# Kernel optimization log

Measured on AMD Instinct MI355X. Metric: run time of the kernel, lower is better.

The kernel has to match this reference:

```python
import jax, jax.numpy as jnp
import numpy as np

B1, B2, R, L, D, H = 48, 48, 36, 30, 1024, 4
EPS = 1e-8


def _l2norm(x):
    return x / (jnp.sqrt(jnp.sum(x * x, axis=-1, keepdims=True)) + EPS)


def _summary_attn(x, w1, b1, w2, b2):
    # x: (B1,B2,N,D). MLP scores -> softmax over N -> weighted mean over H heads.
    h = jax.nn.relu(jnp.einsum('abnd,ed->abne', x, w1) + b1)
    s = jnp.einsum('abne,he->abnh', h, w2) + b2          # (B1,B2,N,H)
    p = jax.nn.softmax(jnp.swapaxes(s, -1, -2), axis=-1)  # (B1,B2,H,N)
    w = jnp.einsum('abhn,abnd->abhd', p, x)               # (B1,B2,H,D)
    return w.mean(axis=-2)                                # (B1,B2,D)


def setup_inputs() -> dict:
    key = jax.random.key(0)
    ks = jax.random.split(key, 12)
    r = np.sqrt(6.0) / np.sqrt(D + D)  # xavier uniform as in init_weights
    return {
        'v1': jax.random.normal(ks[0], (B1, R, D), dtype=jnp.float32),
        'v2': jax.random.normal(ks[1], (B2, L, D), dtype=jnp.float32),
        'w_img': jax.random.uniform(ks[2], (D, D), jnp.float32, -r, r),
        'w_txt': jax.random.uniform(ks[3], (D, D), jnp.float32, -r, r),
        'w1a': jax.random.normal(ks[4], (D, D), jnp.float32) * 0.02,
        'b1a': jnp.zeros((D,), jnp.float32),
        'w2a': jax.random.normal(ks[5], (H, D), jnp.float32) * 0.02,
        'b2a': jnp.zeros((H,), jnp.float32),
        'w1b': jax.random.normal(ks[6], (D, D), jnp.float32) * 0.02,
        'b1b': jnp.zeros((D,), jnp.float32),
        'w2b': jax.random.normal(ks[7], (H, D), jnp.float32) * 0.02,
        'b2b': jnp.zeros((H,), jnp.float32),
    }


def reference(v1, v2, w_img, w_txt, w1a, b1a, w2a, b2a, w1b, b1b, w2b, b2b):
    d = v1.shape[-1]
    inv_sqrt_d = np.float32(1.0 / np.sqrt(d))
    k1 = jnp.einsum('ard,ed->are', v1, w_img)  # (B1,R,D)
    k2 = jnp.einsum('bld,ed->ble', v2, w_txt)  # (B2,L,D)

    # qkv_attention(k2, k1, v1): queries=words, keys/values=regions
    s1 = jnp.einsum('bld,ard->ablr', k2, k1) * inv_sqrt_d   # (B1,B2,L,R)
    p1 = jax.nn.softmax(s1, axis=-1)
    fused_v2 = jnp.einsum('ablr,ard->abld', p1, v1)         # weighted_v1 -> fused_v2

    # qkv_attention(k1, k2, v2): queries=regions, keys/values=words
    s2 = jnp.einsum('ard,bld->abrl', k1, k2) * inv_sqrt_d   # (B1,B2,R,L)
    p2 = jax.nn.softmax(s2, axis=-1)
    fused_v1 = jnp.einsum('abrl,bld->abrd', p2, v2)         # weighted_v2 -> fused_v1

    co_v1 = _l2norm(_summary_attn(fused_v1, w1a, b1a, w2a, b2a))
    co_v2 = _l2norm(_summary_attn(fused_v2, w1b, b1b, w2b, b2b))
    return jnp.sum(co_v1 * co_v2, axis=-1)  # (B1,B2) score matrix
```

## Files before the change

### kernel.cpp

```cpp
#include <hip/hip_runtime.h>

#define D 1024
#define NB1 48
#define NB2 48
#define RR 36
#define LL 30
#define NH 4

typedef short bf16x8 __attribute__((ext_vector_type(8)));
typedef float f32x4 __attribute__((ext_vector_type(4)));
typedef float f32x2 __attribute__((ext_vector_type(2)));
typedef unsigned short u16x8 __attribute__((ext_vector_type(8)));

#define MFMA16(a, b, c) __builtin_amdgcn_mfma_f32_16x16x32_bf16(a, b, c, 0, 0, 0)

__device__ __forceinline__ unsigned short f2bf(float x) {
  unsigned u = __float_as_uint(x);
  u += 0x7FFF + ((u >> 16) & 1);
  return (unsigned short)(u >> 16);
}
__device__ __forceinline__ float bf2f(unsigned short h) {
  return __uint_as_float(((unsigned)h) << 16);
}
__device__ __forceinline__ void split8(const float* v, bf16x8& h8, bf16x8& l8) {
  u16x8 hi, lo;
#pragma unroll
  for (int i = 0; i < 8; ++i) {
    unsigned short h = f2bf(v[i]);
    hi[i] = h;
    lo[i] = f2bf(v[i] - bf2f(h));
  }
  h8 = __builtin_bit_cast(bf16x8, hi);
  l8 = __builtin_bit_cast(bf16x8, lo);
}
__device__ __forceinline__ f32x2 shflx2(f32x2 v, int m) {
  double d = __builtin_bit_cast(double, v);
  d = __shfl_xor(d, m);
  return __builtin_bit_cast(f32x2, d);
}

__device__ __forceinline__ void conv_body(const float* __restrict__ X,
                                          unsigned short* __restrict__ out,
                                          int rows, int g) {
  const int lane = threadIdx.x & 63;
  const int tile = g >> 5, kc = g & 31;
  const int row = tile * 16 + (lane & 15);
  const int k = kc * 32 + (lane >> 4) * 8;
  float v[8];
  if (row < rows) {
    const float4* s = (const float4*)(X + (size_t)row * 1024 + k);
    float4 x0 = s[0], x1 = s[1];
    v[0] = x0.x; v[1] = x0.y; v[2] = x0.z; v[3] = x0.w;
    v[4] = x1.x; v[5] = x1.y; v[6] = x1.z; v[7] = x1.w;
  } else {
#pragma unroll
    for (int i = 0; i < 8; ++i) v[i] = 0.f;
  }
  bf16x8 hi, lo;
  split8(v, hi, lo);
  bf16x8* o = (bf16x8*)(out + (size_t)g * 1024 + lane * 8);
  o[0] = hi;
  o[64] = lo;
}

__global__ __launch_bounds__(256) void conv6(
    const float* __restrict__ v1, const float* __restrict__ v2,
    const float* __restrict__ wimg, const float* __restrict__ wtxt,
    const float* __restrict__ w1a, const float* __restrict__ w1b,
    const float* __restrict__ w2a, const float* __restrict__ w2b,
    unsigned short* v1f, unsigned short* v2f, unsigned short* wimgf,
    unsigned short* wtxtf, unsigned short* w1af, unsigned short* w1bf,
    float4* __restrict__ w2at, float4* __restrict__ w2bt) {
  if (blockIdx.y == 0 && blockIdx.x < 4) {
    int col = blockIdx.x * 256 + threadIdx.x;
    w2at[col] = make_float4(w2a[col], w2a[1024 + col], w2a[2048 + col], w2a[3072 + col]);
    w2bt[col] = make_float4(w2b[col], w2b[1024 + col], w2b[2048 + col], w2b[3072 + col]);
  }
  const float* X; unsigned short* O; int rows;
  switch (blockIdx.y) {
    case 0: X = v1; O = v1f; rows = 1728; break;
    case 1: X = v2; O = v2f; rows = 1440; break;
    case 2: X = wimg; O = wimgf; rows = 1024; break;
    case 3: X = wtxt; O = wtxtf; rows = 1024; break;
    case 4: X = w1a; O = w1af; rows = 1024; break;
    default: X = w1b; O = w1bf; rows = 1024; break;
  }
  const int tiles = (rows + 15) >> 4;
  const int g = blockIdx.x * 4 + (threadIdx.x >> 6);
  if (g >= tiles * 32) return;
  conv_body(X, O, rows, g);
}

__global__ __launch_bounds__(256) void convG(const float* __restrict__ G2a,
                                             const float* __restrict__ G1b,
                                             unsigned short* G2aF,
                                             unsigned short* G1bF) {
  const int t = threadIdx.x, lane = t & 63;
  const int bb = blockIdx.x >> 4;
  const int nt = ((blockIdx.x & 15) << 2) + (t >> 6);
  const int c = lane & 15, q = lane >> 4;
  if (blockIdx.y == 0) {
    float v[8];
#pragma unroll
    for (int j = 0; j < 8; ++j) {
      int l = q * 8 + j;
      v[j] = (l < LL) ? G2a[(size_t)(bb * LL + l) * D + nt * 16 + c] : 0.f;
    }
    bf16x8 hi, lo;
    split8(v, hi, lo);
    bf16x8* o = (bf16x8*)(G2aF + ((size_t)(bb * 64 + nt) * 2) * 512 + lane * 8);
    o[0] = hi;
    o[64] = lo;
  } else {
#pragma unroll
    for (int kc = 0; kc < 2; ++kc) {
      float v[8];
#pragma unroll
      for (int j = 0; j < 8; ++j) {
        int r = kc * 32 + q * 8 + j;
        v[j] = (r < RR) ? G1b[(size_t)(bb * RR + r) * D + nt * 16 + c] : 0.f;
      }
      bf16x8 hi, lo;
      split8(v, hi, lo);
      bf16x8* o = (bf16x8*)(G1bF + (((size_t)(bb * 64 + nt) * 2 + kc) * 2) * 512 + lane * 8);
      o[0] = hi;
      o[64] = lo;
    }
  }
}

#define LOAD_FRAGS(AH, AL, BH, BL)                                              \
  {                                                                             \
    _Pragma("unroll") for (int i = 0; i < 4; ++i) {                             \
      AH[i] = Af[ab[i]]; AL[i] = Af[ab[i] + 64]; ab[i] += 128;                  \
    }                                                                           \
    _Pragma("unroll") for (int j = 0; j < 4; ++j) {                             \
      BH[j] = Bf[bb[j]]; BL[j] = Bf[bb[j] + 64]; bb[j] += 128;                  \
    }                                                                           \
  }

#define MFMA_SET(AH, AL, BH, BL)                                                \
  _Pragma("unroll") for (int i = 0; i < 4; ++i)                                 \
      _Pragma("unroll") for (int j = 0; j < 4; ++j) {                           \
    acc[i][j] = MFMA16(AH[i], BH[j], acc[i][j]);                                \
    acc[i][j] = MFMA16(AL[i], BH[j], acc[i][j]);                                \
    acc[i][j] = MFMA16(AH[i], BL[j], acc[i][j]);                                \
  }

__device__ __forceinline__ void gemm2w_acc(const bf16x8* __restrict__ Af,
                                           const bf16x8* __restrict__ Bf,
                                           int Mtiles, int Ntiles,
                                           int mb, int nb, int lane,
                                           f32x4 (&acc)[4][4]) {
  int ab[4], bb[4];
#pragma unroll
  for (int i = 0; i < 4; ++i) {
    int tm = mb + i; if (tm > Mtiles - 1) tm = Mtiles - 1;
    ab[i] = tm * 4096 + lane;
    int tn = nb + i; if (tn > Ntiles - 1) tn = Ntiles - 1;
    bb[i] = tn * 4096 + lane;
  }
#pragma unroll
  for (int i = 0; i < 4; ++i)
#pragma unroll
    for (int j = 0; j < 4; ++j) acc[i][j] = (f32x4){0.f, 0.f, 0.f, 0.f};

  bf16x8 ahA[4], alA[4], bhA[4], blA[4];
  bf16x8 ahB[4], alB[4], bhB[4], blB[4];
  LOAD_FRAGS(ahA, alA, bhA, blA);
#pragma unroll 1
  for (int kc = 0; kc < 30; kc += 2) {
    LOAD_FRAGS(ahB, alB, bhB, blB);
    MFMA_SET(ahA, alA, bhA, blA);
    LOAD_FRAGS(ahA, alA, bhA, blA);
    MFMA_SET(ahB, alB, bhB, blB);
  }
  LOAD_FRAGS(ahB, alB, bhB, blB);
  MFMA_SET(ahA, alA, bhA, blA);
  MFMA_SET(ahB, alB, bhB, blB);
}

__device__ __forceinline__ void gemm2w_store_fp32(f32x4 (&acc)[4][4],
                                                  float* __restrict__ C,
                                                  int M, int N, float scale,
                                                  int mb, int nb, int lane) {
  const int c16 = lane & 15, q = lane >> 4;
#pragma unroll
  for (int i = 0; i < 4; ++i) {
#pragma unroll
    for (int reg = 0; reg < 4; ++reg) {
      int r = (mb + i) * 16 + q * 4 + reg;
      if (r < M) {
#pragma unroll
        for (int j = 0; j < 4; ++j) {
          int col = (nb + j) * 16 + c16;
          if (col < N) C[(size_t)r * N + col] = acc[i][j][reg] * scale;
        }
      }
    }
  }
}

__global__ __launch_bounds__(128) void proj_fused(
    const bf16x8* __restrict__ v1f, const bf16x8* __restrict__ v2f,
    const bf16x8* __restrict__ wimgf, const bf16x8* __restrict__ wtxtf,
    const bf16x8* __restrict__ w1af, const bf16x8* __restrict__ w1bf,
    float* G2a, float* G1b,
    unsigned short* k1f, unsigned short* k2f) {
  const int z = blockIdx.z;
  const int lane = threadIdx.x & 63;
  const int w = threadIdx.x >> 6;
  const int mb = blockIdx.y * 8 + w * 4;
  const int nb = blockIdx.x * 4;
  const bf16x8* Af = (z == 0 || z == 3) ? v1f : v2f;
  const bf16x8* Bf = (z == 0) ? wimgf : (z == 1) ? wtxtf : (z == 2) ? w1af : w1bf;
  const int Mt = (z == 0 || z == 3) ? 108 : 90;
  if ((int)blockIdx.y * 8 >= Mt) return;

  __shared__ __align__(16) float tlds[2][4][16][68];

  f32x4 acc[4][4];
  gemm2w_acc(Af, Bf, Mt, 64, mb, nb, lane, acc);

  if (z <= 1) {
    unsigned short* F = z ? k2f : k1f;
    const int c16 = lane & 15, q = lane >> 4;
#pragma unroll
    for (int i = 0; i < 4; ++i)
#pragma unroll
      for (int j = 0; j < 4; ++j)
#pragma unroll
        for (int reg = 0; reg < 4; ++reg)
          tlds[w][i][q * 4 + reg][j * 16 + c16] = acc[i][j][reg];
    __builtin_amdgcn_sched_barrier(0);
    const int r16 = lane & 15, q2 = lane >> 4;
#pragma unroll
    for (int i = 0; i < 4; ++i) {
      if (mb + i < Mt) {
#pragma unroll
        for (int kcl = 0; kcl < 2; ++kcl) {
          const float* rp = &tlds[w][i][r16][kcl * 32 + q2 * 8];
          float4 x0 = *(const float4*)rp;
          float4 x1 = *(const float4*)(rp + 4);
          float v[8];
          v[0] = x0.x; v[1] = x0.y; v[2] = x0.z; v[3] = x0.w;
          v[4] = x1.x; v[5] = x1.y; v[6] = x1.z; v[7] = x1.w;
          bf16x8 hi, lo;
          split8(v, hi, lo);
          size_t g = (size_t)(mb + i) * 32 + (nb >> 1) + kcl;
          bf16x8* o = (bf16x8*)(F + g * 1024 + lane * 8);
          o[0] = hi;
          o[64] = lo;
        }
      }
    }
  } else {
    float* C = (z == 2) ? G2a : G1b;
    const int M = (z == 2) ? 1440 : 1728;
    gemm2w_store_fp32(acc, C, M, 1024, 1.f, mb, nb, lane);
  }
}

__global__ __launch_bounds__(128) void cross_s(
    const bf16x8* __restrict__ k2f, const bf16x8* __restrict__ k1f,
    float* Sbuf) {
  const int lane = threadIdx.x & 63;
  const int w = threadIdx.x >> 6;
  const int mb = blockIdx.y * 8 + w * 4;
  const int nb = blockIdx.x * 4;
  f32x4 acc[4][4];
  gemm2w_acc(k2f, k1f, 90, 108, mb, nb, lane, acc);
  gemm2w_store_fp32(acc, Sbuf, 1440, 1728, 0.03125f, mb, nb, lane);
}

__global__ __launch_bounds__(256, 4) void pair_dir(
    const float* __restrict__ Sb,
    const bf16x8* __restrict__ G2aF, const bf16x8* __restrict__ G1bF,
    const float* __restrict__ b1a, const float4* __restrict__ w2at, const float* __restrict__ b2a,
    const float* __restrict__ b1b, const float4* __restrict__ w2bt, const float* __restrict__ b2b,
    float* __restrict__ U1buf, float* __restrict__ U2buf) {
  const int t = threadIdx.x, lane = t & 63, w = t >> 6;
  const int bx = blockIdx.x;
  int a, b, dir;
  if (bx < 576) {
    dir = 0;
    const int lo = bx & 7, i = bx >> 3;
    b = lo + 8 * (i % 6);
    a = (i / 6) * 4 + w;
  } else {
    dir = 1;
    const int bx2 = bx - 576;
    const int lo = bx2 & 7, i = bx2 >> 3;
    a = lo + 8 * (i % 6);
    b = (i / 6) * 4 + w;
  }
  const int c16 = lane & 15, q = lane >> 4;

  union WSM {
    struct { float p2s[36][36]; float sa[36][NH]; float qa[36]; } A;
    struct { float p1s[30][36]; float sbm[30][NH]; float qb[30]; } B;
  };
  __shared__ __align__(16) WSM sm[4];
  WSM& S = sm[w];

  const float* Sab = Sb + (size_t)(b * LL) * 1728 + a * RR;

  if (dir == 0) {
    if (lane < RR) { S.A.p2s[lane][30] = 0.f; S.A.p2s[lane][31] = 0.f; }
    __builtin_amdgcn_sched_barrier(0);
    for (int i = lane; i < LL * RR; i += 64) {
      int l = i / RR, r = i - l * RR;
      S.A.p2s[r][l] = Sab[(size_t)l * 1728 + r];
    }
    __builtin_amdgcn_sched_barrier(0);
    if (lane < RR) {
      const int r = lane;
      float m = -1e30f;
      for (int l = 0; l < LL; ++l) m = fmaxf(m, S.A.p2s[r][l]);
      float s = 0.f;
      for (int l = 0; l < LL; ++l) {
        float e = __expf(S.A.p2s[r][l] - m);
        S.A.p2s[r][l] = e;
        s += e;
      }
      float inv = 1.f / s;
      for (int l = 0; l < LL; ++l) S.A.p2s[r][l] *= inv;
    }
    __builtin_amdgcn_sched_barrier(0);

    bf16x8 pAh[3], pAl[3];
#pragma unroll
    for (int mt = 0; mt < 3; ++mt) {
      int rr = mt * 16 + c16;
      if (rr > RR - 1) rr = RR - 1;
      float v[8];
      const float* rp = &S.A.p2s[rr][q * 8];
      float4 x0 = *(const float4*)rp;
      float4 x1 = *(const float4*)(rp + 4);
      v[0] = x0.x; v[1] = x0.y; v[2] = x0.z; v[3] = x0.w;
      v[4] = x1.x; v[5] = x1.y; v[6] = x1.z; v[7] = x1.w;
      split8(v, pAh[mt], pAl[mt]);
    }

    f32x2 sc01[3][4], sc23[3][4];
#pragma unroll
    for (int mt = 0; mt < 3; ++mt)
#pragma unroll
      for (int reg = 0; reg < 4; ++reg) {
        sc01[mt][reg] = (f32x2){0.f, 0.f};
        sc23[mt][reg] = (f32x2){0.f, 0.f};
      }

    const bf16x8* gA = G2aF + (size_t)(b * 64) * 128 + lane;
#pragma unroll 2
    for (int it = 0; it < 64; ++it) {
      const bf16x8* gp = gA + (size_t)it * 128;
      bf16x8 Bh = gp[0], Bl = gp[64];
      const int col = it * 16 + c16;
      float4 wv = w2at[col];
      float bias = b1a[col];
      f32x2 w01 = {wv.x, wv.y}, w23 = {wv.z, wv.w};
#pragma unroll
      for (int mt = 0; mt < 3; ++mt) {
        f32x4 acc = {bias, bias, bias, bias};
        __builtin_amdgcn_s_setprio(1);
        acc = MFMA16(pAh[mt], Bh, acc);
        acc = MFMA16(pAl[mt], Bh, acc);
        acc = MFMA16(pAh[mt], Bl, acc);
        __builtin_amdgcn_s_setprio(0);
#pragma unroll
        for (int reg = 0; reg < 4; ++reg) {
          float hv = fmaxf(acc[reg], 0.f);
          f32x2 hv2 = {hv, hv};
          sc01[mt][reg] += hv2 * w01;
          sc23[mt][reg] += hv2 * w23;
        }
      }
    }
    f32x2 b01 = {b2a[0], b2a[1]}, b23 = {b2a[2], b2a[3]};
#pragma unroll
    for (int mt = 0; mt < 3; ++mt)
#pragma unroll
      for (int reg = 0; reg < 4; ++reg) {
        f32x2 v01 = sc01[mt][reg], v23 = sc23[mt][reg];
#pragma unroll
        for (int m = 1; m <= 8; m <<= 1) {
          v01 += shflx2(v01, m);
          v23 += shflx2(v23, m);
        }
        int row = mt * 16 + q * 4 + reg;
        if (c16 == 0 && row < RR) {
          f32x2* rp = (f32x2*)&S.A.sa[row][0];
          rp[0] = v01 + b01;
          rp[1] = v23 + b23;
        }
      }
    __builtin_amdgcn_sched_barrier(0);
    {
      const int h = q, i = c16;
      float x0 = S.A.sa[i][h];
      float x1 = S.A.sa[i + 16][h];
      float x2 = (i < 4) ? S.A.sa[i + 32][h] : -1e30f;
      float m = fmaxf(fmaxf(x0, x1), x2);
      m = fmaxf(m, __shfl_xor(m, 1));
      m = fmaxf(m, __shfl_xor(m, 2));
      m = fmaxf(m, __shfl_xor(m, 4));
      m = fmaxf(m, __shfl_xor(m, 8));
      float e0 = __expf(x0 - m), e1 = __expf(x1 - m);
      float e2 = (i < 4) ? __expf(x2 - m) : 0.f;
      float s = e0 + e1 + e2;
      s += __shfl_xor(s, 1);
      s += __shfl_xor(s, 2);
      s += __shfl_xor(s, 4);
      s += __shfl_xor(s, 8);
      float inv = 0.25f / s;
      float p0 = e0 * inv, p1 = e1 * inv, p2v = e2 * inv;
      p0 += __shfl_xor(p0, 16); p0 += __shfl_xor(p0, 32);
      p1 += __shfl_xor(p1, 16); p1 += __shfl_xor(p1, 32);
      p2v += __shfl_xor(p2v, 16); p2v += __shfl_xor(p2v, 32);
      if (q == 0) {
        S.A.qa[i] = p0;
        S.A.qa[i + 16] = p1;
        if (i < 4) S.A.qa[i + 32] = p2v;
      }
    }
    __builtin_amdgcn_sched_barrier(0);
    if (lane < LL) {
      const int l = lane;
      float x = 0.f;
      for (int r = 0; r < RR; ++r) x = fmaf(S.A.qa[r], S.A.p2s[r][l], x);
      U2buf[((size_t)b * 48 + a) * 32 + l] = x;
    }
  } else {
    for (int i = lane; i < LL * RR; i += 64) {
      int l = i / RR, r = i - l * RR;
      S.B.p1s[l][r] = Sab[(size_t)l * 1728 + r];
    }
    __builtin_amdgcn_sched_barrier(0);
    if (lane < LL) {
      const int l = lane;
      float m = -1e30f;
      for (int r = 0; r < RR; ++r) m = fmaxf(m, S.B.p1s[l][r]);
      float s = 0.f;
      for (int r = 0; r < RR; ++r) {
        float e = __expf(S.B.p1s[l][r] - m);
        S.B.p1s[l][r] = e;
        s += e;
      }
      float inv = 1.f / s;
      for (int r = 0; r < RR; ++r) S.B.p1s[l][r] *= inv;
    }
    __builtin_amdgcn_sched_barrier(0);

    bf16x8 pBh[2][2], pBl[2][2];
#pragma unroll
    for (int mt = 0; mt < 2; ++mt) {
      int rr = mt * 16 + c16;
      if (rr > LL - 1) rr = LL - 1;
      {
        float v[8];
        const float* rp = &S.B.p1s[rr][q * 8];
        float4 x0 = *(const float4*)rp;
        float4 x1 = *(const float4*)(rp + 4);
        v[0] = x0.x; v[1] = x0.y; v[2] = x0.z; v[3] = x0.w;
        v[4] = x1.x; v[5] = x1.y; v[6] = x1.z; v[7] = x1.w;
        split8(v, pBh[mt][0], pBl[mt][0]);
      }
      {
        float v[8];
#pragma unroll
        for (int j = 0; j < 8; ++j) {
          int r = 32 + q * 8 + j;
          v[j] = (r < RR) ? S.B.p1s[rr][r] : 0.f;
        }
        split8(v, pBh[mt][1], pBl[mt][1]);
      }
    }

    f32x2 sc01[2][4], sc23[2][4];
#pragma unroll
    for (int mt = 0; mt < 2; ++mt)
#pragma unroll
      for (int reg = 0; reg < 4; ++reg) {
        sc01[mt][reg] = (f32x2){0.f, 0.f};
        sc23[mt][reg] = (f32x2){0.f, 0.f};
      }

    const bf16x8* gB = G1bF + (size_t)(a * 64) * 256 + lane;
#pragma unroll 2
    for (int it = 0; it < 64; ++it) {
      const bf16x8* gp = gB + (size_t)it * 256;
      bf16x8 B0h = gp[0], B0l = gp[64], B1h = gp[128], B1l = gp[192];
      const int col = it * 16 + c16;
      float4 wv = w2bt[col];
      float bias = b1b[col];
      f32x2 w01 = {wv.x, wv.y}, w23 = {wv.z, wv.w};
#pragma unroll
      for (int mt = 0; mt < 2; ++mt) {
        f32x4 acc = {bias, bias, bias, bias};
        __builtin_amdgcn_s_setprio(1);
        acc = MFMA16(pBh[mt][0], B0h, acc);
        acc = MFMA16(pBl[mt][0], B0h, acc);
        acc = MFMA16(pBh[mt][0], B0l, acc);
        acc = MFMA16(pBh[mt][1], B1h, acc);
        acc = MFMA16(pBl[mt][1], B1h, acc);
        acc = MFMA16(pBh[mt][1], B1l, acc);
        __builtin_amdgcn_s_setprio(0);
#pragma unroll
        for (int reg = 0; reg < 4; ++reg) {
          float hv = fmaxf(acc[reg], 0.f);
          f32x2 hv2 = {hv, hv};
          sc01[mt][reg] += hv2 * w01;
          sc23[mt][reg] += hv2 * w23;
        }
      }
    }
    f32x2 b01 = {b2b[0], b2b[1]}, b23 = {b2b[2], b2b[3]};
#pragma unroll
    for (int mt = 0; mt < 2; ++mt)
#pragma unroll
      for (int reg = 0; reg < 4; ++reg) {
        f32x2 v01 = sc01[mt][reg], v23 = sc23[mt][reg];
#pragma unroll
        for (int m = 1; m <= 8; m <<= 1) {
          v01 += shflx2(v01, m);
          v23 += shflx2(v23, m);
        }
        int row = mt * 16 + q * 4 + reg;
        if (c16 == 0 && row < LL) {
          f32x2* rp = (f32x2*)&S.B.sbm[row][0];
          rp[0] = v01 + b01;
          rp[1] = v23 + b23;
        }
      }
    __builtin_amdgcn_sched_barrier(0);
    {
      const int h = q, i = c16;
      float x0 = S.B.sbm[i][h];
      float x1 = (i < 14) ? S.B.sbm[i + 16][h] : -1e30f;
      float m = fmaxf(x0, x1);
      m = fmaxf(m, __shfl_xor(m, 1));
      m = fmaxf(m, __shfl_xor(m, 2));
      m = fmaxf(m, __shfl_xor(m, 4));
      m = fmaxf(m, __shfl_xor(m, 8));
      float e0 = __expf(x0 - m);
      float e1 = (i < 14) ? __expf(x1 - m) : 0.f;
      float s = e0 + e1;
      s += __shfl_xor(s, 1);
      s += __shfl_xor(s, 2);
      s += __shfl_xor(s, 4);
      s += __shfl_xor(s, 8);
      float inv = 0.25f / s;
      float p0 = e0 * inv, p1 = e1 * inv;
      p0 += __shfl_xor(p0, 16); p0 += __shfl_xor(p0, 32);
      p1 += __shfl_xor(p1, 16); p1 += __shfl_xor(p1, 32);
      if (q == 0) {
        S.B.qb[i] = p0;
        if (i < 14) S.B.qb[i + 16] = p1;
      }
    }
    __builtin_amdgcn_sched_barrier(0);
    if (lane < RR) {
      const int r = lane;
      float x = 0.f;
      for (int l = 0; l < LL; ++l) x = fmaf(S.B.qb[l], S.B.p1s[l][r], x);
      U1buf[((size_t)a * 48 + b) * 40 + r] = x;
    }
  }
}

__global__ __launch_bounds__(256) void y_batch(
    const float* __restrict__ v1, const float* __restrict__ v2,
    const float* __restrict__ U1buf, const float* __restrict__ U2buf,
    float* __restrict__ YA, float* __restrict__ YB) {
  const int bb = blockIdx.x;
  const int col = blockIdx.z * 256 + threadIdx.x;
  __shared__ float us[48 * 40];
  float y[48];
#pragma unroll
  for (int i = 0; i < 48; ++i) y[i] = 0.f;
  if (blockIdx.y == 0) {
    for (int i = threadIdx.x; i < 48 * 32; i += 256) us[i] = U2buf[(size_t)bb * 1536 + i];
    __syncthreads();
    const float* V = v2 + (size_t)bb * LL * 1024 + col;
    for (int l = 0; l < LL; ++l) {
      float v = V[(size_t)l * 1024];
#pragma unroll
      for (int i = 0; i < 48; ++i) y[i] = fmaf(us[i * 32 + l], v, y[i]);
    }
    float* Yo = YA + (size_t)bb * 48 * 1024 + col;
#pragma unroll
    for (int i = 0; i < 48; ++i) Yo[(size_t)i * 1024] = y[i];
  } else {
    for (int i = threadIdx.x; i < 48 * 40; i += 256) us[i] = U1buf[(size_t)bb * 1920 + i];
    __syncthreads();
    const float* V = v1 + (size_t)bb * RR * 1024 + col;
    for (int r = 0; r < RR; ++r) {
      float v = V[(size_t)r * 1024];
#pragma unroll
      for (int i = 0; i < 48; ++i) y[i] = fmaf(us[i * 40 + r], v, y[i]);
    }
    float* Yo = YB + (size_t)bb * 48 * 1024 + col;
#pragma unroll
    for (int i = 0; i < 48; ++i) Yo[(size_t)i * 1024] = y[i];
  }
}

__global__ __launch_bounds__(256) void pair_final(
    const float* __restrict__ YA, const float* __restrict__ YB,
    float* __restrict__ out) {
  const int pair = blockIdx.x;
  const int a = pair / NB2;
  const int b = pair - a * NB2;
  const int t = threadIdx.x;
  const float4* ya = (const float4*)(YA + ((size_t)b * 48 + a) * 1024);
  const float4* yb = (const float4*)(YB + ((size_t)a * 48 + b) * 1024);
  float4 va = ya[t], vb = yb[t];
  float num = va.x * vb.x + va.y * vb.y + va.z * vb.z + va.w * vb.w;
  float n1 = va.x * va.x + va.y * va.y + va.z * va.z + va.w * va.w;
  float n2 = vb.x * vb.x + vb.y * vb.y + vb.z * vb.z + vb.w * vb.w;
#pragma unroll
  for (int off = 32; off; off >>= 1) {
    num += __shfl_down(num, off);
    n1 += __shfl_down(n1, off);
    n2 += __shfl_down(n2, off);
  }
  __shared__ float r3[3][4];
  if ((t & 63) == 0) {
    r3[0][t >> 6] = num; r3[1][t >> 6] = n1; r3[2][t >> 6] = n2;
  }
  __syncthreads();
  if (t == 0) {
    float nu = r3[0][0] + r3[0][1] + r3[0][2] + r3[0][3];
    float s1 = sqrtf(fmaxf(r3[1][0] + r3[1][1] + r3[1][2] + r3[1][3], 0.f));
    float s2 = sqrtf(fmaxf(r3[2][0] + r3[2][1] + r3[2][2] + r3[2][3], 0.f));
    out[pair] = nu / ((s1 + 1e-8f) * (s2 + 1e-8f));
  }
}

extern "C" void kernel_launch(void* const* d_in, const int* in_sizes, int n_in,
                              void* d_out, int out_size, void* d_ws, size_t ws_size,
                              hipStream_t stream) {
  const float* v1    = (const float*)d_in[0];
  const float* v2    = (const float*)d_in[1];
  const float* w_img = (const float*)d_in[2];
  const float* w_txt = (const float*)d_in[3];
  const float* w1a   = (const float*)d_in[4];
  const float* b1a   = (const float*)d_in[5];
  const float* w2a   = (const float*)d_in[6];
  const float* b2a   = (const float*)d_in[7];
  const float* w1b   = (const float*)d_in[8];
  const float* b1b   = (const float*)d_in[9];
  const float* w2b   = (const float*)d_in[10];
  const float* b2b   = (const float*)d_in[11];
  float* out = (float*)d_out;

  float* ws   = (float*)d_ws;
  float* k1   = ws;
  float* k2   = k1 + (size_t)1728 * 1024;
  float* G2a  = k2 + (size_t)1440 * 1024;
  float* G1b  = G2a + (size_t)1440 * 1024;
  float* Sbuf = G1b + (size_t)1728 * 1024;
  float* Cbuf = Sbuf + (size_t)1440 * 1728;
  float* g22  = Cbuf + (size_t)1440 * 1728;
  float* g11  = g22 + (size_t)48 * 900;
  (void)k1; (void)k2;

  unsigned short* fb    = (unsigned short*)(g11 + (size_t)48 * 1296);
  unsigned short* v1f   = fb;
  unsigned short* v2f   = v1f + (size_t)108 * 32768;
  unsigned short* k1f   = v2f + (size_t)92 * 32768;
  unsigned short* k2f   = k1f + (size_t)108 * 32768;
  unsigned short* wimgf = k2f + (size_t)92 * 32768;
  unsigned short* wtxtf = wimgf + (size_t)64 * 32768;
  unsigned short* w1af  = wtxtf + (size_t)64 * 32768;
  unsigned short* w1bf  = w1af + (size_t)64 * 32768;
  unsigned short* G2aF  = w1bf + (size_t)64 * 32768;
  unsigned short* G1bF  = G2aF + (size_t)48 * 65536;

  float4* w2at = (float4*)g22;
  float4* w2bt = w2at + 1024;

  float* U2buf = G2a;
  float* U1buf = U2buf + (size_t)48 * 48 * 32;
  float* YA = Cbuf;
  float* YB = (float*)k1f;

  conv6<<<dim3(864, 6), 256, 0, stream>>>(v1, v2, w_img, w_txt, w1a, w1b,
                                          w2a, w2b,
                                          v1f, v2f, wimgf, wtxtf, w1af, w1bf,
                                          w2at, w2bt);

  proj_fused<<<dim3(16, 14, 4), 128, 0, stream>>>(
      (const bf16x8*)v1f, (const bf16x8*)v2f, (const bf16x8*)wimgf,
      (const bf16x8*)wtxtf, (const bf16x8*)w1af, (const bf16x8*)w1bf,
      G2a, G1b, k1f, k2f);

  cross_s<<<dim3(27, 12), 128, 0, stream>>>(
      (const bf16x8*)k2f, (const bf16x8*)k1f, Sbuf);

  convG<<<dim3(768, 2), 256, 0, stream>>>(G2a, G1b, G2aF, G1bF);

  pair_dir<<<1152, 256, 0, stream>>>(
      Sbuf, (const bf16x8*)G2aF, (const bf16x8*)G1bF,
      b1a, w2at, b2a, b1b, w2bt, b2b, U1buf, U2buf);
  y_batch<<<dim3(48, 2, 4), 256, 0, stream>>>(v1, v2, U1buf, U2buf, YA, YB);
  pair_final<<<2304, 256, 0, stream>>>(YA, YB, out);
}
```

Before: 284.3 us.

## Move G projections out of projK and run them alongside the cross-score GEMM

Splits the fused projection kernel so the first launch only computes the k1/k2 projections. The G2a/G1b GEMMs, which do not depend on k1/k2, move into a second launch that also computes the cross-score S GEMM. This shortens the critical path: the S GEMM no longer waits behind the G GEMMs and shares a launch with them, filling the device better. The cost is a combined grid (27x14x3) in which many blocks exit early, plus some branch overhead.

```diff
diff --git a/kernel.cpp b/kernel.cpp
--- a/kernel.cpp
+++ b/kernel.cpp
@@ -201,20 +201,18 @@
   }
 }
 
-__global__ __launch_bounds__(128) void proj_fused(
+__global__ __launch_bounds__(128) void projK(
     const bf16x8* __restrict__ v1f, const bf16x8* __restrict__ v2f,
     const bf16x8* __restrict__ wimgf, const bf16x8* __restrict__ wtxtf,
-    const bf16x8* __restrict__ w1af, const bf16x8* __restrict__ w1bf,
-    float* G2a, float* G1b,
     unsigned short* k1f, unsigned short* k2f) {
   const int z = blockIdx.z;
   const int lane = threadIdx.x & 63;
   const int w = threadIdx.x >> 6;
   const int mb = blockIdx.y * 8 + w * 4;
   const int nb = blockIdx.x * 4;
-  const bf16x8* Af = (z == 0 || z == 3) ? v1f : v2f;
-  const bf16x8* Bf = (z == 0) ? wimgf : (z == 1) ? wtxtf : (z == 2) ? w1af : w1bf;
-  const int Mt = (z == 0 || z == 3) ? 108 : 90;
+  const bf16x8* Af = (z == 0) ? v1f : v2f;
+  const bf16x8* Bf = (z == 0) ? wimgf : wtxtf;
+  const int Mt = (z == 0) ? 108 : 90;
   if ((int)blockIdx.y * 8 >= Mt) return;
 
   __shared__ __align__(16) float tlds[2][4][16][68];
@@ -222,55 +220,67 @@
   f32x4 acc[4][4];
   gemm2w_acc(Af, Bf, Mt, 64, mb, nb, lane, acc);
 
-  if (z <= 1) {
-    unsigned short* F = z ? k2f : k1f;
-    const int c16 = lane & 15, q = lane >> 4;
-#pragma unroll
-    for (int i = 0; i < 4; ++i)
-#pragma unroll
-      for (int j = 0; j < 4; ++j)
-#pragma unroll
-        for (int reg = 0; reg < 4; ++reg)
-          tlds[w][i][q * 4 + reg][j * 16 + c16] = acc[i][j][reg];
-    __builtin_amdgcn_sched_barrier(0);
-    const int r16 = lane & 15, q2 = lane >> 4;
-#pragma unroll
-    for (int i = 0; i < 4; ++i) {
-      if (mb + i < Mt) {
-#pragma unroll
-        for (int kcl = 0; kcl < 2; ++kcl) {
-          const float* rp = &tlds[w][i][r16][kcl * 32 + q2 * 8];
-          float4 x0 = *(const float4*)rp;
-          float4 x1 = *(const float4*)(rp + 4);
-          float v[8];
-          v[0] = x0.x; v[1] = x0.y; v[2] = x0.z; v[3] = x0.w;
-          v[4] = x1.x; v[5] = x1.y; v[6] = x1.z; v[7] = x1.w;
-          bf16x8 hi, lo;
-          split8(v, hi, lo);
-          size_t g = (size_t)(mb + i) * 32 + (nb >> 1) + kcl;
-          bf16x8* o = (bf16x8*)(F + g * 1024 + lane * 8);
-          o[0] = hi;
-          o[64] = lo;
-        }
-      }
-    }
-  } else {
-    float* C = (z == 2) ? G2a : G1b;
-    const int M = (z == 2) ? 1440 : 1728;
-    gemm2w_store_fp32(acc, C, M, 1024, 1.f, mb, nb, lane);
-  }
-}
-
-__global__ __launch_bounds__(128) void cross_s(
+  unsigned short* F = z ? k2f : k1f;
+  const int c16 = lane & 15, q = lane >> 4;
+#pragma unroll
+  for (int i = 0; i < 4; ++i)
+#pragma unroll
+    for (int j = 0; j < 4; ++j)
+#pragma unroll
+      for (int reg = 0; reg < 4; ++reg)
+        tlds[w][i][q * 4 + reg][j * 16 + c16] = acc[i][j][reg];
+  __builtin_amdgcn_sched_barrier(0);
+  const int r16 = lane & 15, q2 = lane >> 4;
+#pragma unroll
+  for (int i = 0; i < 4; ++i) {
+    if (mb + i < Mt) {
+#pragma unroll
+      for (int kcl = 0; kcl < 2; ++kcl) {
+        const float* rp = &tlds[w][i][r16][kcl * 32 + q2 * 8];
+        float4 x0 = *(const float4*)rp;
+        float4 x1 = *(const float4*)(rp + 4);
+        float v[8];
+        v[0] = x0.x; v[1] = x0.y; v[2] = x0.z; v[3] = x0.w;
+        v[4] = x1.x; v[5] = x1.y; v[6] = x1.z; v[7] = x1.w;
+        bf16x8 hi, lo;
+        split8(v, hi, lo);
+        size_t g = (size_t)(mb + i) * 32 + (nb >> 1) + kcl;
+        bf16x8* o = (bf16x8*)(F + g * 1024 + lane * 8);
+        o[0] = hi;
+        o[64] = lo;
+      }
+    }
+  }
+}
+
+__global__ __launch_bounds__(128) void projG_cross(
+    const bf16x8* __restrict__ v1f, const bf16x8* __restrict__ v2f,
+    const bf16x8* __restrict__ w1af, const bf16x8* __restrict__ w1bf,
     const bf16x8* __restrict__ k2f, const bf16x8* __restrict__ k1f,
-    float* Sbuf) {
+    float* G2a, float* G1b, float* Sbuf) {
+  const int z = blockIdx.z;
   const int lane = threadIdx.x & 63;
   const int w = threadIdx.x >> 6;
+  f32x4 acc[4][4];
+  if (z == 2) {
+    if (blockIdx.x >= 27 || blockIdx.y >= 12) return;
+    const int mb = blockIdx.y * 8 + w * 4;
+    const int nb = blockIdx.x * 4;
+    gemm2w_acc(k2f, k1f, 90, 108, mb, nb, lane, acc);
+    gemm2w_store_fp32(acc, Sbuf, 1440, 1728, 0.03125f, mb, nb, lane);
+    return;
+  }
+  if (blockIdx.x >= 16) return;
+  const bf16x8* Af = (z == 0) ? v2f : v1f;
+  const bf16x8* Bf = (z == 0) ? w1af : w1bf;
+  float* C = (z == 0) ? G2a : G1b;
+  const int Mt = (z == 0) ? 90 : 108;
+  const int M = (z == 0) ? 1440 : 1728;
+  if ((int)blockIdx.y * 8 >= Mt) return;
   const int mb = blockIdx.y * 8 + w * 4;
   const int nb = blockIdx.x * 4;
-  f32x4 acc[4][4];
-  gemm2w_acc(k2f, k1f, 90, 108, mb, nb, lane, acc);
-  gemm2w_store_fp32(acc, Sbuf, 1440, 1728, 0.03125f, mb, nb, lane);
+  gemm2w_acc(Af, Bf, Mt, 64, mb, nb, lane, acc);
+  gemm2w_store_fp32(acc, C, M, 1024, 1.f, mb, nb, lane);
 }
 
 __global__ __launch_bounds__(256, 4) void pair_dir(
@@ -691,13 +701,15 @@
                                           v1f, v2f, wimgf, wtxtf, w1af, w1bf,
                                           w2at, w2bt);
 
-  proj_fused<<<dim3(16, 14, 4), 128, 0, stream>>>(
+  projK<<<dim3(16, 14, 2), 128, 0, stream>>>(
       (const bf16x8*)v1f, (const bf16x8*)v2f, (const bf16x8*)wimgf,
-      (const bf16x8*)wtxtf, (const bf16x8*)w1af, (const bf16x8*)w1bf,
-      G2a, G1b, k1f, k2f);
-
-  cross_s<<<dim3(27, 12), 128, 0, stream>>>(
-      (const bf16x8*)k2f, (const bf16x8*)k1f, Sbuf);
+      (const bf16x8*)wtxtf, k1f, k2f);
+
+  projG_cross<<<dim3(27, 14, 3), 128, 0, stream>>>(
+      (const bf16x8*)v1f, (const bf16x8*)v2f,
+      (const bf16x8*)w1af, (const bf16x8*)w1bf,
+      (const bf16x8*)k2f, (const bf16x8*)k1f,
+      G2a, G1b, Sbuf);
 
   convG<<<dim3(768, 2), 256, 0, stream>>>(G2a, G1b, G2aF, G1bF);
 
```

Measured after the change: 302.9 us. 6.6% more time.
